# Kernel optimization log

Hardware: AMD Instinct MI355X
Metric: run time of the kernel (lower is better)

## Reference

```python
import jax, jax.numpy as jnp
import numpy as np

N, S, D = 512, 64, 128   # num_nodes, seq_len, model_size
H, K = 4, 32             # num_heads, key_size
E = 4096                 # num_edges
WF = 4                   # widening_factor
EPS = 1e-5


def _alibi(num_heads, seq_len):
    slopes = 2.0 ** (-8.0 * (jnp.arange(1, num_heads + 1, dtype=jnp.float32) / num_heads))
    pos = jnp.arange(seq_len, dtype=jnp.float32)
    rel = pos[None, :] - pos[:, None]  # T - t, <= 0 in causal region
    return (slopes[:, None, None] * rel)[None]  # [1,H,S,S]


def layer_norm(x, scale, offset):
    mu = jnp.mean(x, axis=-1, keepdims=True)
    var = jnp.var(x, axis=-1, keepdims=True)
    return (x - mu) * jax.lax.rsqrt(var + EPS) * scale + offset


def segment_softmax(logits, seg, num_segments):
    maxs = jax.ops.segment_max(logits, seg, num_segments=num_segments)
    e = jnp.exp(logits - maxs[seg])
    denom = jax.ops.segment_sum(e, seg, num_segments=num_segments)
    return e / denom[seg]


def setup_inputs() -> dict:
    key = jax.random.key(0)
    ks = jax.random.split(key, 24)
    sd = 0.02
    inp = {
        'nodes': jax.random.normal(ks[0], (N, S, D), jnp.float32),
        'senders': jax.random.randint(ks[1], (E,), 0, N, jnp.int32),
        'receivers': jax.random.randint(ks[2], (E,), 0, N, jnp.int32),
        'alibi_mask': _alibi(H, S),
        'ln1_s': jnp.ones((D,)), 'ln1_b': jnp.zeros((D,)),
        'wq': jax.random.normal(ks[3], (D, H * K)) * sd, 'bq': jnp.zeros((H * K,)),
        'wk': jax.random.normal(ks[4], (D, H * K)) * sd, 'bk': jnp.zeros((H * K,)),
        'wv': jax.random.normal(ks[5], (D, H * K)) * sd, 'bv': jnp.zeros((H * K,)),
        'wo': jax.random.normal(ks[6], (H * K, D)) * sd, 'bo': jnp.zeros((D,)),
        'ln2_s': jnp.ones((D,)), 'ln2_b': jnp.zeros((D,)),
        'w1': jax.random.normal(ks[7], (D, WF * D)) * sd, 'b1': jnp.zeros((WF * D,)),
        'w2': jax.random.normal(ks[8], (WF * D, D)) * sd, 'b2': jnp.zeros((D,)),
        'ln3_s': jnp.ones((D,)), 'ln3_b': jnp.zeros((D,)),
        'w_sa': jax.random.normal(ks[9], (2 * D, D)) * sd, 'b_sa': jnp.zeros((D,)),
        'w_sq': jax.random.normal(ks[10], (D, H * D)) * sd, 'b_sq': jnp.zeros((H * D,)),
    }
    return inp


def reference(nodes, senders, receivers, alibi_mask,
              ln1_s, ln1_b, wq, bq, wk, bk, wv, bv, wo, bo,
              ln2_s, ln2_b, w1, b1, w2, b2, ln3_s, ln3_b,
              w_sa, b_sa, w_sq, b_sq):
    n, s, d = nodes.shape
    # --- node self-attention with ALiBi + causal mask ---
    xn = layer_norm(nodes, ln1_s, ln1_b)
    q = (xn @ wq + bq).reshape(n, s, H, K)
    k = (xn @ wk + bk).reshape(n, s, H, K)
    v = (xn @ wv + bv).reshape(n, s, H, K)
    logits = jnp.einsum('nthk,nThk->nhtT', q, k)
    logits = alibi_mask + logits / jnp.sqrt(jnp.float32(K))
    causal = jnp.tril(jnp.ones((1, 1, s, s), dtype=bool))
    logits = jnp.where(causal, logits, -1e30)
    w = jax.nn.softmax(logits, axis=-1)
    attn = jnp.einsum('nhtT,nThk->nthk', w, v).reshape(n, s, H * K)
    nodes = nodes + (attn @ wo + bo)  # dropout rate 0 (eval)
    # --- FFN block ---
    xn = layer_norm(nodes, ln2_s, ln2_b)
    dense = jax.nn.gelu(xn @ w1 + b1) @ w2 + b2
    nodes = layer_norm(nodes + dense, ln3_s, ln3_b)
    # --- graph message passing: gather / segment-softmax / segment-sum ---
    sent = nodes[senders]        # [E,S,D]
    recv = nodes[receivers]      # [E,S,D]
    sl = jnp.concatenate([sent, recv], axis=-1) @ w_sa + b_sa  # [E,S,D]
    aw = segment_softmax(sl, receivers, n)                     # [E,S,D]
    sq = (aw @ w_sq + b_sq).reshape(E, s, H, d)                # [E,S,H,D]
    messages = jnp.mean(sq * sent[:, :, None, :], axis=2)      # [E,S,D]
    out = jax.ops.segment_sum(messages, receivers, num_segments=n)
    return out
```

## Files before the change

### kernel.cpp

```cpp
#include <hip/hip_runtime.h>
#include <hip/hip_bf16.h>

typedef __hip_bfloat16 bf16;
typedef __attribute__((ext_vector_type(8))) __bf16 bf8v;
typedef __attribute__((ext_vector_type(4))) float  f4v;

#define NN 512
#define SSEQ 64
#define DDIM 128
#define HH 4
#define NROWS (NN*SSEQ)
#define EMAX 4096
#define ECH 64

__device__ __forceinline__ float b2f(bf16 x){ return __bfloat162float(x); }
__device__ __forceinline__ bf16 f2b(float x){ return __float2bfloat16(x); }
__device__ __forceinline__ float ldf(float x){ return x; }
__device__ __forceinline__ float ldf(bf16 x){ return b2f(x); }
__device__ __forceinline__ void stf(float* p, float v){ *p = v; }
__device__ __forceinline__ void stf(bf16* p, float v){ *p = f2b(v); }

__device__ __forceinline__ f4v mfma16(bf8v a, bf8v b, f4v c){
  return __builtin_amdgcn_mfma_f32_16x16x32_bf16(a, b, c, 0, 0, 0);
}
__device__ __forceinline__ bf8v ldfrag(const void* p){
  return __builtin_bit_cast(bf8v, *(const int4*)p);
}
__device__ __forceinline__ float gelu_f(float v){
  return 0.5f*v*(1.0f + tanhf(0.7978845608028654f*(v + 0.044715f*v*v*v)));
}

__global__ __launch_bounds__(512) void prep_all_k(
    const float* wq, const float* wk, const float* wv, const float* wo,
    const float* w1, const float* w2, const float* wsa,
    const float* w_sq, const float* b_sq,
    const float* bq, const float* bk, const float* bv,
    const int* __restrict__ receivers,
    bf16* wqkvT, bf16* woT, bf16* w1T, bf16* w2T, bf16* wsaTt,
    bf16* wbarT, float* bbar, float* qkv_bias,
    int* off, int* perm, int* chunk_cnt, int E){
  int b = blockIdx.x, t = threadIdx.x;
  if (b < 832){
    if (t >= 256) return;
    const float* W; bf16* Wt; int K, lN, rel, roff = 0;
    if      (b < 64) { W=wq;  Wt=wqkvT; K=128; lN=7; rel=b;     roff=0;   }
    else if (b <128) { W=wk;  Wt=wqkvT; K=128; lN=7; rel=b-64;  roff=128; }
    else if (b <192) { W=wv;  Wt=wqkvT; K=128; lN=7; rel=b-128; roff=256; }
    else if (b <256) { W=wo;  Wt=woT;   K=128; lN=7; rel=b-192; }
    else if (b <512) { W=w1;  Wt=w1T;   K=128; lN=9; rel=b-256; }
    else if (b <768) { W=w2;  Wt=w2T;   K=512; lN=7; rel=b-512; }
    else             { W=wsa; Wt=wsaTt; K=128; lN=7; rel=b-768; }
    int i = rel*256 + t;
    int k = i >> lN, n = i & ((1<<lN)-1);
    Wt[(size_t)(n+roff)*K + k] = f2b(W[i]);
  } else if (b < 896){
    if (t >= 256) return;
    int i = (b-832)*256 + t;
    int c = i>>7, d = i&127;
    float s = 0.f;
    #pragma unroll
    for (int h=0;h<HH;++h) s += w_sq[(size_t)c*(HH*DDIM) + h*DDIM + d];
    wbarT[d*DDIM + c] = f2b(0.25f*s);
  } else if (b < 898){
    if (t >= 256) return;
    int idx = (b-896)*256 + t;
    if (idx < 128){
      float s = 0.f;
      #pragma unroll
      for (int h=0;h<HH;++h) s += b_sq[h*DDIM + idx];
      bbar[idx] = 0.25f*s;
    } else if (idx < 512){
      int j = idx - 128;
      float v = (j<128) ? bq[j] : (j<256) ? bk[j-128] : bv[j-256];
      qkv_bias[j] = v;
    }
  } else if (b == 898){
    __shared__ int s_cnt[NN];
    s_cnt[t] = 0;
    __syncthreads();
    for (int e=t; e<E; e+=512) atomicAdd(&s_cnt[receivers[e]], 1);
    __syncthreads();
    int deg = s_cnt[t];
    int acc = 0, myrank = 0;
    for (int i=0;i<NN;++i){
      int di = s_cnt[i];
      acc    += (i<t) ? di : 0;
      myrank += ((di > deg) || (di == deg && i < t)) ? 1 : 0;
    }
    off[t] = acc;
    if (t==NN-1) off[NN] = acc + deg;
    perm[myrank] = t;
  } else {
    __shared__ int hc[NN];
    int c = b - 899;
    for (int i=t;i<NN;i+=512) hc[i]=0;
    __syncthreads();
    if (t < ECH){
      int e = c*ECH + t;
      if (e < E) atomicAdd(&hc[receivers[e]], 1);
    }
    __syncthreads();
    for (int i=t;i<NN;i+=512) chunk_cnt[(size_t)c*NN + i] = hc[i];
  }
}

__global__ __launch_bounds__(512) void base_k(const int* __restrict__ off,
    const int* __restrict__ chunk_cnt, int* __restrict__ base, int nch){
  int n = threadIdx.x;
  int run = off[n];
  for (int c=0;c<nch;++c){
    base[(size_t)c*NN + n] = run;
    run += chunk_cnt[(size_t)c*NN + n];
  }
}

__global__ __launch_bounds__(64) void slot_k(const int* __restrict__ senders,
    const int* __restrict__ receivers, const int* __restrict__ base,
    int* __restrict__ slot_snd, int E){
  int t = threadIdx.x, c = blockIdx.x;
  int e = c*ECH + t;
  bool valid = (e < E);
  int r  = valid ? receivers[e] : -1;
  int sd = valid ? senders[e]   : 0;
  int rank = 0;
  #pragma unroll
  for (int i=0;i<64;++i){
    int ri = __shfl(r, i);
    rank += (i < t && ri == r) ? 1 : 0;
  }
  if (valid) slot_snd[base[(size_t)c*NN + r] + rank] = sd;
}

template<typename TIN, typename TOUT>
__global__ __launch_bounds__(256) void ln_k(const TIN* __restrict__ x,
    const float* __restrict__ sc, const float* __restrict__ of,
    TOUT* __restrict__ y){
  int row  = blockIdx.x*4 + (threadIdx.x>>6);
  int lane = threadIdx.x & 63;
  size_t base = (size_t)row*DDIM;
  float v0 = ldf(x[base+lane]);
  float v1 = ldf(x[base+lane+64]);
  float s = v0+v1, q = v0*v0+v1*v1;
  #pragma unroll
  for (int m=1;m<64;m<<=1){ s += __shfl_xor(s,m); q += __shfl_xor(q,m); }
  float mu   = s*(1.0f/DDIM);
  float var  = q*(1.0f/DDIM) - mu*mu;
  float rstd = rsqrtf(var + 1e-5f);
  stf(&y[base+lane],    (v0-mu)*rstd*sc[lane]    + of[lane]);
  stf(&y[base+lane+64], (v1-mu)*rstd*sc[lane+64] + of[lane+64]);
}

template<int KT, int ACT, typename TR, bool RES, bool BIAS>
__global__ __launch_bounds__(256) void gemm_m(const bf16* __restrict__ A,
    const bf16* __restrict__ Wt, const float* __restrict__ bias,
    const TR* __restrict__ R, bf16* __restrict__ C, int N){
  __shared__ bf16 sA[64][72];
  __shared__ bf16 sB[64][72];
  int t = threadIdx.x;
  int bm = blockIdx.x, bn = blockIdx.y;
  int w = t>>6, lane = t&63;
  int wr = w>>1, wc = w&1;
  f4v acc[2][2] = {};
  for (int ks=0; ks<KT; ks+=64){
    #pragma unroll
    for (int p=0;p<2;++p){
      int r = p*32 + (t>>3), cc = (t&7)*8;
      *(int4*)(&sA[r][cc]) = *(const int4*)(A  + (size_t)(bm*64+r)*KT + ks + cc);
      *(int4*)(&sB[r][cc]) = *(const int4*)(Wt + (size_t)(bn*64+r)*KT + ks + cc);
    }
    __syncthreads();
    #pragma unroll
    for (int k0=0;k0<64;k0+=32){
      int kc = k0 + 8*(lane>>4);
      bf8v a0 = ldfrag(&sA[wr*32      + (lane&15)][kc]);
      bf8v a1 = ldfrag(&sA[wr*32 + 16 + (lane&15)][kc]);
      bf8v b0 = ldfrag(&sB[wc*32      + (lane&15)][kc]);
      bf8v b1 = ldfrag(&sB[wc*32 + 16 + (lane&15)][kc]);
      acc[0][0] = mfma16(a0, b0, acc[0][0]);
      acc[0][1] = mfma16(a0, b1, acc[0][1]);
      acc[1][0] = mfma16(a1, b0, acc[1][0]);
      acc[1][1] = mfma16(a1, b1, acc[1][1]);
    }
    __syncthreads();
  }
  #pragma unroll
  for (int j=0;j<2;++j){
    int gcol = bn*64 + wc*32 + j*16 + (lane&15);
    float bs = BIAS ? bias[gcol] : 0.f;
    #pragma unroll
    for (int i=0;i<2;++i){
      #pragma unroll
      for (int r=0;r<4;++r){
        int grow = bm*64 + wr*32 + i*16 + 4*(lane>>4) + r;
        float v = acc[i][j][r] + bs;
        if (ACT==1) v = gelu_f(v);
        if (ACT==2) v = __expf(v);
        if (RES) v += ldf(R[(size_t)grow*N + gcol]);
        C[(size_t)grow*N + gcol] = f2b(v);
      }
    }
  }
}

__global__ __launch_bounds__(256) void gemm_wo_ln2_k(const bf16* __restrict__ A,
    const bf16* __restrict__ Wt, const float* __restrict__ bias,
    const float* __restrict__ Rres, const float* __restrict__ lns,
    const float* __restrict__ lnb, bf16* __restrict__ n2out,
    bf16* __restrict__ xnout){
  __shared__ bf16 sA[64][72];
  __shared__ bf16 sB[128][72];
  __shared__ float s_st[2][2][32][2];
  int t = threadIdx.x, bm = blockIdx.x;
  int w = t>>6, lane = t&63, ls = lane&15, lg = lane>>4;
  int wr = w>>1, wc = w&1;
  f4v acc[2][4] = {};
  for (int ks=0; ks<128; ks+=64){
    #pragma unroll
    for (int p=0;p<2;++p){
      int r = p*32 + (t>>3), cc = (t&7)*8;
      *(int4*)(&sA[r][cc]) = *(const int4*)(A + (size_t)(bm*64+r)*128 + ks + cc);
    }
    #pragma unroll
    for (int p=0;p<4;++p){
      int r = p*32 + (t>>3), cc = (t&7)*8;
      *(int4*)(&sB[r][cc]) = *(const int4*)(Wt + (size_t)r*128 + ks + cc);
    }
    __syncthreads();
    #pragma unroll
    for (int k0=0;k0<64;k0+=32){
      int kc = k0 + 8*lg;
      bf8v a0 = ldfrag(&sA[wr*32      + ls][kc]);
      bf8v a1 = ldfrag(&sA[wr*32 + 16 + ls][kc]);
      #pragma unroll
      for (int j=0;j<4;++j){
        bf8v bj = ldfrag(&sB[wc*64 + j*16 + ls][kc]);
        acc[0][j] = mfma16(a0, bj, acc[0][j]);
        acc[1][j] = mfma16(a1, bj, acc[1][j]);
      }
    }
    __syncthreads();
  }
  float x[2][4][4];
  float psum[2][4], psq[2][4];
  #pragma unroll
  for (int i=0;i<2;++i)
    #pragma unroll
    for (int r=0;r<4;++r){ psum[i][r]=0.f; psq[i][r]=0.f; }
  #pragma unroll
  for (int i=0;i<2;++i){
    #pragma unroll
    for (int j=0;j<4;++j){
      int col = wc*64 + j*16 + ls;
      float bs = bias[col];
      #pragma unroll
      for (int r=0;r<4;++r){
        int row = bm*64 + wr*32 + i*16 + 4*lg + r;
        float v = acc[i][j][r] + bs + Rres[(size_t)row*128 + col];
        x[i][j][r] = v;
        psum[i][r] += v;
        psq[i][r]  += v*v;
        n2out[(size_t)row*128 + col] = f2b(v);
      }
    }
  }
  #pragma unroll
  for (int i=0;i<2;++i)
    #pragma unroll
    for (int r=0;r<4;++r){
      float s_=psum[i][r], q_=psq[i][r];
      s_ += __shfl_xor(s_,1); s_ += __shfl_xor(s_,2);
      s_ += __shfl_xor(s_,4); s_ += __shfl_xor(s_,8);
      q_ += __shfl_xor(q_,1); q_ += __shfl_xor(q_,2);
      q_ += __shfl_xor(q_,4); q_ += __shfl_xor(q_,8);
      if (ls == 0){
        int rl = i*16 + 4*lg + r;
        s_st[wr][wc][rl][0] = s_;
        s_st[wr][wc][rl][1] = q_;
      }
    }
  __syncthreads();
  #pragma unroll
  for (int i=0;i<2;++i){
    #pragma unroll
    for (int r=0;r<4;++r){
      int rl = i*16 + 4*lg + r;
      float s_ = s_st[wr][0][rl][0] + s_st[wr][1][rl][0];
      float q_ = s_st[wr][0][rl][1] + s_st[wr][1][rl][1];
      float mu = s_*(1.0f/DDIM);
      float var = q_*(1.0f/DDIM) - mu*mu;
      float rstd = rsqrtf(var + 1e-5f);
      int row = bm*64 + wr*32 + rl;
      #pragma unroll
      for (int j=0;j<4;++j){
        int col = wc*64 + j*16 + ls;
        xnout[(size_t)row*128 + col] = f2b((x[i][j][r]-mu)*rstd*lns[col] + lnb[col]);
      }
    }
  }
}

__global__ __launch_bounds__(256) void gemm_w2_tail_k(const bf16* __restrict__ A,
    const bf16* __restrict__ Wt, const float* __restrict__ bias,
    const bf16* __restrict__ Rres, const float* __restrict__ lns,
    const float* __restrict__ lnb, const bf16* __restrict__ wsaT,
    bf16* __restrict__ r2out, bf16* __restrict__ yexpout){
  __shared__ bf16 sA[64][72];
  __shared__ bf16 sB[128][72];
  __shared__ bf16 sY[64][136];
  __shared__ float s_st[2][2][32][2];
  int t = threadIdx.x, bm = blockIdx.x;
  int w = t>>6, lane = t&63, ls = lane&15, lg = lane>>4;
  int wr = w>>1, wc = w&1;
  f4v acc[2][4] = {};
  for (int ks=0; ks<512; ks+=64){
    #pragma unroll
    for (int p=0;p<2;++p){
      int r = p*32 + (t>>3), cc = (t&7)*8;
      *(int4*)(&sA[r][cc]) = *(const int4*)(A + (size_t)(bm*64+r)*512 + ks + cc);
    }
    #pragma unroll
    for (int p=0;p<4;++p){
      int r = p*32 + (t>>3), cc = (t&7)*8;
      *(int4*)(&sB[r][cc]) = *(const int4*)(Wt + (size_t)r*512 + ks + cc);
    }
    __syncthreads();
    #pragma unroll
    for (int k0=0;k0<64;k0+=32){
      int kc = k0 + 8*lg;
      bf8v a0 = ldfrag(&sA[wr*32      + ls][kc]);
      bf8v a1 = ldfrag(&sA[wr*32 + 16 + ls][kc]);
      #pragma unroll
      for (int j=0;j<4;++j){
        bf8v bj = ldfrag(&sB[wc*64 + j*16 + ls][kc]);
        acc[0][j] = mfma16(a0, bj, acc[0][j]);
        acc[1][j] = mfma16(a1, bj, acc[1][j]);
      }
    }
    __syncthreads();
  }
  float x[2][4][4];
  float psum[2][4], psq[2][4];
  #pragma unroll
  for (int i=0;i<2;++i)
    #pragma unroll
    for (int r=0;r<4;++r){ psum[i][r]=0.f; psq[i][r]=0.f; }
  #pragma unroll
  for (int i=0;i<2;++i){
    #pragma unroll
    for (int j=0;j<4;++j){
      int col = wc*64 + j*16 + ls;
      float bs = bias[col];
      #pragma unroll
      for (int r=0;r<4;++r){
        int row = bm*64 + wr*32 + i*16 + 4*lg + r;
        float v = acc[i][j][r] + bs + b2f(Rres[(size_t)row*128 + col]);
        x[i][j][r] = v;
        psum[i][r] += v;
        psq[i][r]  += v*v;
      }
    }
  }
  #pragma unroll
  for (int i=0;i<2;++i)
    #pragma unroll
    for (int r=0;r<4;++r){
      float s_=psum[i][r], q_=psq[i][r];
      s_ += __shfl_xor(s_,1); s_ += __shfl_xor(s_,2);
      s_ += __shfl_xor(s_,4); s_ += __shfl_xor(s_,8);
      q_ += __shfl_xor(q_,1); q_ += __shfl_xor(q_,2);
      q_ += __shfl_xor(q_,4); q_ += __shfl_xor(q_,8);
      if (ls == 0){
        int rl = i*16 + 4*lg + r;
        s_st[wr][wc][rl][0] = s_;
        s_st[wr][wc][rl][1] = q_;
      }
    }
  __syncthreads();
  #pragma unroll
  for (int i=0;i<2;++i){
    #pragma unroll
    for (int r=0;r<4;++r){
      int rl = i*16 + 4*lg + r;
      float s_ = s_st[wr][0][rl][0] + s_st[wr][1][rl][0];
      float q_ = s_st[wr][0][rl][1] + s_st[wr][1][rl][1];
      float mu = s_*(1.0f/DDIM);
      float var = q_*(1.0f/DDIM) - mu*mu;
      float rstd = rsqrtf(var + 1e-5f);
      int row = bm*64 + wr*32 + rl;
      #pragma unroll
      for (int j=0;j<4;++j){
        int col = wc*64 + j*16 + ls;
        bf16 yb = f2b((x[i][j][r]-mu)*rstd*lns[col] + lnb[col]);
        r2out[(size_t)row*128 + col] = yb;
        sY[wr*32 + rl][col] = yb;
      }
    }
  }
  __syncthreads();
  f4v acc2[2][4] = {};
  for (int ks2=0; ks2<128; ks2+=64){
    #pragma unroll
    for (int p=0;p<4;++p){
      int r = p*32 + (t>>3), cc = (t&7)*8;
      *(int4*)(&sB[r][cc]) = *(const int4*)(wsaT + (size_t)r*128 + ks2 + cc);
    }
    __syncthreads();
    #pragma unroll
    for (int k0=0;k0<64;k0+=32){
      int kc = k0 + 8*lg;
      bf8v a0 = ldfrag(&sY[wr*32      + ls][ks2 + kc]);
      bf8v a1 = ldfrag(&sY[wr*32 + 16 + ls][ks2 + kc]);
      #pragma unroll
      for (int j=0;j<4;++j){
        bf8v bj = ldfrag(&sB[wc*64 + j*16 + ls][kc]);
        acc2[0][j] = mfma16(a0, bj, acc2[0][j]);
        acc2[1][j] = mfma16(a1, bj, acc2[1][j]);
      }
    }
    __syncthreads();
  }
  #pragma unroll
  for (int i=0;i<2;++i){
    #pragma unroll
    for (int j=0;j<4;++j){
      int col = wc*64 + j*16 + ls;
      #pragma unroll
      for (int r=0;r<4;++r){
        int row = bm*64 + wr*32 + i*16 + 4*lg + r;
        yexpout[(size_t)row*128 + col] = f2b(__expf(acc2[i][j][r]));
      }
    }
  }
}

__global__ __launch_bounds__(256) void attn_m(const bf16* __restrict__ qkvb,
    bf16* __restrict__ ob){
  __shared__ bf16 sVT[128][72];
  __shared__ bf16 sP[4][64][72];
  int t = threadIdx.x, n = blockIdx.x;
  int w = t>>6, lane = t&63, ls = lane&15, lg = lane>>4;
  const bf16* qbase = qkvb + (size_t)n*SSEQ*(3*DDIM);
  bf8v qf[4], kf[4];
  #pragma unroll
  for (int mi=0;mi<4;++mi)
    qf[mi] = ldfrag(qbase + (size_t)(16*mi + ls)*(3*DDIM) + 32*w + 8*lg);
  #pragma unroll
  for (int ni=0;ni<4;++ni)
    kf[ni] = ldfrag(qbase + (size_t)(16*ni + ls)*(3*DDIM) + DDIM + 32*w + 8*lg);
  for (int id = t; id < 1024; id += 256){
    int T = id>>4, c = id&15;
    int4 v = *(const int4*)(qbase + (size_t)T*(3*DDIM) + 2*DDIM + c*8);
    const bf16* pv = (const bf16*)&v;
    #pragma unroll
    for (int j=0;j<8;++j){
      int d = c*8 + j;
      sVT[d][T ^ (((d>>3)&7)<<3)] = pv[j];
    }
  }
  f4v accS[4][4];
  #pragma unroll
  for (int mi=0;mi<4;++mi)
    #pragma unroll
    for (int ni=0;ni<4;++ni){
      f4v z = {};
      accS[mi][ni] = mfma16(qf[mi], kf[ni], z);
    }
  __syncthreads();
  const float scale = 0.17677669529663687f;
  const float slope = 1.0f / (float)(4 << (2*w));
  float den[4][4];
  #pragma unroll
  for (int mi=0;mi<4;++mi)
    #pragma unroll
    for (int r=0;r<4;++r) den[mi][r] = 0.f;
  #pragma unroll
  for (int mi=0;mi<4;++mi){
    #pragma unroll
    for (int ni=0;ni<4;++ni){
      #pragma unroll
      for (int r=0;r<4;++r){
        int rel = (16*ni + ls) - (16*mi + 4*lg + r);
        float p = (rel <= 0) ? __expf(accS[mi][ni][r]*scale + slope*(float)rel) : 0.f;
        accS[mi][ni][r] = p;
        den[mi][r] += p;
      }
    }
  }
  #pragma unroll
  for (int mi=0;mi<4;++mi)
    #pragma unroll
    for (int r=0;r<4;++r){
      float d_ = den[mi][r];
      d_ += __shfl_xor(d_, 1);  d_ += __shfl_xor(d_, 2);
      d_ += __shfl_xor(d_, 4);  d_ += __shfl_xor(d_, 8);
      den[mi][r] = 1.0f / d_;
    }
  #pragma unroll
  for (int mi=0;mi<4;++mi)
    #pragma unroll
    for (int ni=0;ni<4;++ni)
      #pragma unroll
      for (int r=0;r<4;++r)
        sP[w][16*mi + 4*lg + r][16*ni + ls] = f2b(accS[mi][ni][r]*den[mi][r]);
  f4v oacc[4][2] = {};
  #pragma unroll
  for (int ks=0;ks<2;++ks){
    bf8v vf[2];
    #pragma unroll
    for (int ni2=0;ni2<2;++ni2){
      int d = 32*w + 16*ni2 + ls;
      vf[ni2] = ldfrag(&sVT[d][(32*ks + 8*lg) ^ (((d>>3)&7)<<3)]);
    }
    #pragma unroll
    for (int mi=0;mi<4;++mi){
      bf8v pa = ldfrag(&sP[w][16*mi + ls][32*ks + 8*lg]);
      #pragma unroll
      for (int ni2=0;ni2<2;++ni2)
        oacc[mi][ni2] = mfma16(pa, vf[ni2], oacc[mi][ni2]);
    }
  }
  #pragma unroll
  for (int mi=0;mi<4;++mi)
    #pragma unroll
    for (int ni2=0;ni2<2;++ni2)
      #pragma unroll
      for (int r=0;r<4;++r)
        ob[(size_t)(n*SSEQ + 16*mi + 4*lg + r)*DDIM + 32*w + 16*ni2 + ls]
          = f2b(oacc[mi][ni2][r]);
}

__global__ __launch_bounds__(128) void msg4_k(const bf16* __restrict__ yexp,
    const bf16* __restrict__ nodes3, const int* __restrict__ off,
    const int* __restrict__ slot_snd, const int* __restrict__ perm,
    const bf16* __restrict__ wbarT, const float* __restrict__ bbar,
    float* __restrict__ out){
  __shared__ bf16  s_sent[2][3][16][72];
  __shared__ float s_den[16][132];
  int t = threadIdx.x, sc = blockIdx.y;
  int n = perm[blockIdx.x];
  int w = t>>6, lane = t&63, ls = lane&15, lg = lane>>4;
  int off0 = off[n], deg = off[n+1]-off0;
  int srow = sc*16 + ls;
  if (deg == 0){
    #pragma unroll
    for (int ct=0;ct<4;++ct)
      #pragma unroll
      for (int r=0;r<4;++r)
        out[((size_t)n*SSEQ + sc*16 + 4*lg + r)*DDIM + w*64 + ct*16 + ls] = 0.f;
    return;
  }
  bf8v B[4][4];
  #pragma unroll
  for (int ct=0;ct<4;++ct)
    #pragma unroll
    for (int kb=0;kb<4;++kb)
      B[ct][kb] = ldfrag(wbarT + (size_t)(w*64 + ct*16 + ls)*DDIM + kb*32 + lg*8);
  float bb[4];
  #pragma unroll
  for (int ct=0;ct<4;++ct) bb[ct] = bbar[w*64 + ct*16 + ls];
  float den[4][8];
  #pragma unroll
  for (int kb=0;kb<4;++kb)
    #pragma unroll
    for (int j=0;j<8;++j) den[kb][j] = 0.f;
  {
    int k = w;
    for (; k+2 < deg; k += 4){
      int s0 = slot_snd[off0+k], s1 = slot_snd[off0+k+2];
      const bf16* y0 = yexp + ((size_t)s0*SSEQ + srow)*DDIM + lg*8;
      const bf16* y1 = yexp + ((size_t)s1*SSEQ + srow)*DDIM + lg*8;
      int4 v0[4], v1[4];
      #pragma unroll
      for (int kb=0;kb<4;++kb) v0[kb] = *(const int4*)(y0 + kb*32);
      #pragma unroll
      for (int kb=0;kb<4;++kb) v1[kb] = *(const int4*)(y1 + kb*32);
      #pragma unroll
      for (int kb=0;kb<4;++kb){
        const bf16* a = (const bf16*)&v0[kb];
        const bf16* b = (const bf16*)&v1[kb];
        #pragma unroll
        for (int j=0;j<8;++j) den[kb][j] += b2f(a[j]) + b2f(b[j]);
      }
    }
    if (k < deg){
      int s0 = slot_snd[off0+k];
      const bf16* y0 = yexp + ((size_t)s0*SSEQ + srow)*DDIM + lg*8;
      #pragma unroll
      for (int kb=0;kb<4;++kb){
        int4 v = *(const int4*)(y0 + kb*32);
        const bf16* a = (const bf16*)&v;
        #pragma unroll
        for (int j=0;j<8;++j) den[kb][j] += b2f(a[j]);
      }
    }
  }
  int l0 = lane*2, l1 = lane*2 + 1;
  int r0 = l0>>3, c0 = (l0&7)*8;
  int r1 = l1>>3, c1 = (l1&7)*8;
  int4 yvA[4], yvB[4], yvC[4];
  {
    int snd = slot_snd[off0];
    const bf16* yr = yexp + ((size_t)snd*SSEQ + srow)*DDIM + lg*8;
    #pragma unroll
    for (int kb=0;kb<4;++kb) yvA[kb] = *(const int4*)(yr + kb*32);
    const bf16* sp = nodes3 + ((size_t)snd*SSEQ + sc*16)*DDIM + w*64;
    *(int4*)&s_sent[w][0][r0][c0] = *(const int4*)(sp + (size_t)r0*DDIM + c0);
    *(int4*)&s_sent[w][0][r1][c1] = *(const int4*)(sp + (size_t)r1*DDIM + c1);
  }
  if (deg > 1){
    int snd = slot_snd[off0+1];
    const bf16* yr = yexp + ((size_t)snd*SSEQ + srow)*DDIM + lg*8;
    #pragma unroll
    for (int kb=0;kb<4;++kb) yvB[kb] = *(const int4*)(yr + kb*32);
    const bf16* sp = nodes3 + ((size_t)snd*SSEQ + sc*16)*DDIM + w*64;
    *(int4*)&s_sent[w][1][r0][c0] = *(const int4*)(sp + (size_t)r0*DDIM + c0);
    *(int4*)&s_sent[w][1][r1][c1] = *(const int4*)(sp + (size_t)r1*DDIM + c1);
  }
  #pragma unroll
  for (int kb=0;kb<4;++kb) yvC[kb] = yvA[kb];
  if (w == 1){
    #pragma unroll
    for (int kb=0;kb<4;++kb)
      #pragma unroll
      for (int j=0;j<8;++j)
        s_den[ls][kb*32 + lg*8 + j] = den[kb][j];
  }
  __syncthreads();
  if (w == 0){
    #pragma unroll
    for (int kb=0;kb<4;++kb)
      #pragma unroll
      for (int j=0;j<8;++j){
        int c = kb*32 + lg*8 + j;
        den[kb][j] = 1.0f / (den[kb][j] + s_den[ls][c]);
        s_den[ls][c] = den[kb][j];
      }
  }
  __syncthreads();
  if (w == 1){
    #pragma unroll
    for (int kb=0;kb<4;++kb)
      #pragma unroll
      for (int j=0;j<8;++j)
        den[kb][j] = s_den[ls][kb*32 + lg*8 + j];
  }
  f4v oacc[4] = {};
  for (int k=0;k<deg;++k){
    if (k+2 < deg){
      int snd2 = slot_snd[off0+k+2];
      const bf16* yr2 = yexp + ((size_t)snd2*SSEQ + srow)*DDIM + lg*8;
      #pragma unroll
      for (int kb=0;kb<4;++kb) yvC[kb] = *(const int4*)(yr2 + kb*32);
      const bf16* sp = nodes3 + ((size_t)snd2*SSEQ + sc*16)*DDIM + w*64;
      int buf2 = (k+2)%3;
      *(int4*)&s_sent[w][buf2][r0][c0] = *(const int4*)(sp + (size_t)r0*DDIM + c0);
      *(int4*)&s_sent[w][buf2][r1][c1] = *(const int4*)(sp + (size_t)r1*DDIM + c1);
    }
    bf8v af[4];
    #pragma unroll
    for (int kb=0;kb<4;++kb){
      const bf16* xv = (const bf16*)&yvA[kb];
      __bf16 tmp[8];
      #pragma unroll
      for (int j=0;j<8;++j){
        bf16 hb_ = f2b(b2f(xv[j]) * den[kb][j]);
        tmp[j] = *(__bf16*)&hb_;
      }
      af[kb] = *(bf8v*)tmp;
    }
    f4v g[4] = {};
    #pragma unroll
    for (int kb=0;kb<4;++kb)
      #pragma unroll
      for (int ct=0;ct<4;++ct)
        g[ct] = mfma16(af[kb], B[ct][kb], g[ct]);
    int buf = k%3;
    #pragma unroll
    for (int ct=0;ct<4;++ct)
      #pragma unroll
      for (int r=0;r<4;++r){
        float sent = b2f(s_sent[w][buf][4*lg + r][ct*16 + ls]);
        oacc[ct][r] += (g[ct][r] + bb[ct]) * sent;
      }
    #pragma unroll
    for (int kb=0;kb<4;++kb){ yvA[kb] = yvB[kb]; yvB[kb] = yvC[kb]; }
  }
  #pragma unroll
  for (int ct=0;ct<4;++ct)
    #pragma unroll
    for (int r=0;r<4;++r)
      out[((size_t)n*SSEQ + sc*16 + 4*lg + r)*DDIM + w*64 + ct*16 + ls] = oacc[ct][r];
}

extern "C" void kernel_launch(void* const* d_in, const int* in_sizes, int n_in,
                              void* d_out, int out_size, void* d_ws, size_t ws_size,
                              hipStream_t stream){
  const float* nodes = (const float*)d_in[0];
  const int*  senders   = (const int*)d_in[1];
  const int*  receivers = (const int*)d_in[2];
  const float* ln1_s=(const float*)d_in[4];  const float* ln1_b=(const float*)d_in[5];
  const float* wq=(const float*)d_in[6];     const float* bq=(const float*)d_in[7];
  const float* wk=(const float*)d_in[8];     const float* bk=(const float*)d_in[9];
  const float* wv=(const float*)d_in[10];    const float* bv_=(const float*)d_in[11];
  const float* wo=(const float*)d_in[12];    const float* bo=(const float*)d_in[13];
  const float* ln2_s=(const float*)d_in[14]; const float* ln2_b=(const float*)d_in[15];
  const float* w1=(const float*)d_in[16];    const float* b1=(const float*)d_in[17];
  const float* w2=(const float*)d_in[18];    const float* b2=(const float*)d_in[19];
  const float* ln3_s=(const float*)d_in[20]; const float* ln3_b=(const float*)d_in[21];
  const float* w_sa=(const float*)d_in[22];
  const float* w_sq=(const float*)d_in[24];  const float* b_sq=(const float*)d_in[25];
  int E = in_sizes[1];
  int nch = (E + ECH - 1)/ECH;

  const size_t MB = 1024*1024;
  char* ws = (char*)d_ws;
  bf16* xn      = (bf16*)(ws);
  bf16* qkvb    = (bf16*)(ws +  8*MB);
  bf16* n2      = (bf16*)(ws + 32*MB);
  bf16* xn2     = (bf16*)(ws + 48*MB);
  bf16* hb      = (bf16*)(ws);
  bf16* attnout = xn;
  bf16* r2     = (bf16*)(ws + 64*MB);
  bf16* yexp   = (bf16*)(ws + 72*MB);
  char* tail = ws + 88*MB;
  bf16*  wbarT   = (bf16*)tail;                       tail += DDIM*DDIM*2;
  float* bbar    = (float*)tail;                      tail += DDIM*4 + 512;
  float* qkv_bias= (float*)tail;                      tail += 3*DDIM*4;
  int*   off     = (int*)tail;                        tail += (NN+8)*4;
  int*   slot_snd= (int*)tail;                        tail += EMAX*4;
  int*   perm    = (int*)tail;                        tail += NN*4;
  int*   ccnt    = (int*)tail;                        tail += 64*NN*4;
  int*   cbase   = (int*)tail;                        tail += 64*NN*4;
  bf16*  wqkvT   = (bf16*)tail;                       tail += 384*128*2;
  bf16*  woT     = (bf16*)tail;                       tail += 128*128*2;
  bf16*  w1T     = (bf16*)tail;                       tail += 128*512*2;
  bf16*  w2T     = (bf16*)tail;                       tail += 512*128*2;
  bf16*  wsaTt   = (bf16*)tail;                       tail += 128*128*2;

  prep_all_k<<<899+nch,512,0,stream>>>(wq,wk,wv,wo,w1,w2,w_sa,w_sq,b_sq,bq,bk,bv_,
                                       receivers,
                                       wqkvT,woT,w1T,w2T,wsaTt,wbarT,bbar,qkv_bias,
                                       off, perm, ccnt, E);
  base_k<<<1,512,0,stream>>>(off, ccnt, cbase, nch);
  slot_k<<<nch,64,0,stream>>>(senders, receivers, cbase, slot_snd, E);

  ln_k<float,bf16><<<NROWS/4,256,0,stream>>>(nodes, ln1_s, ln1_b, xn);
  gemm_m<128,0,float,false,true><<<dim3(NROWS/64,6),256,0,stream>>>(xn, wqkvT, qkv_bias, (const float*)nullptr, qkvb, 384);
  attn_m<<<NN,256,0,stream>>>(qkvb, attnout);
  gemm_wo_ln2_k<<<NROWS/64,256,0,stream>>>(attnout, woT, bo, nodes, ln2_s, ln2_b, n2, xn2);
  gemm_m<128,1,bf16,false,true><<<dim3(NROWS/64,8),256,0,stream>>>(xn2, w1T, b1, (const bf16*)nullptr, hb, 512);
  gemm_w2_tail_k<<<NROWS/64,256,0,stream>>>(hb, w2T, b2, n2, ln3_s, ln3_b, wsaTt, r2, yexp);

  msg4_k<<<dim3(NN,4),128,0,stream>>>(yexp, r2, off, slot_snd, perm, wbarT, bbar, (float*)d_out);
}
```

Measured before the change: 168.5 us.

## Split message kernel across four waves with shared normalized-score tile

The message-passing kernel now runs 256 threads per block. Each of the four waves owns 32 output columns instead of 64, which cuts per-thread weight fragments and accumulators. Each thread loads and normalizes one 8-element slice of the 16x128 score tile per edge and stages it in double-buffered shared memory, replacing per-wave redundant 128-wide row loads. The denominator is computed cooperatively with no cross-wave reduction. The cost is a block-wide barrier every edge iteration and more threads per block.

```diff
diff --git a/kernel.cpp b/kernel.cpp
--- a/kernel.cpp
+++ b/kernel.cpp
@@ -529,167 +529,122 @@
           = f2b(oacc[mi][ni2][r]);
 }
 
-__global__ __launch_bounds__(128) void msg4_k(const bf16* __restrict__ yexp,
+__global__ __launch_bounds__(256) void msg4_k(const bf16* __restrict__ yexp,
     const bf16* __restrict__ nodes3, const int* __restrict__ off,
     const int* __restrict__ slot_snd, const int* __restrict__ perm,
     const bf16* __restrict__ wbarT, const float* __restrict__ bbar,
     float* __restrict__ out){
-  __shared__ bf16  s_sent[2][3][16][72];
-  __shared__ float s_den[16][132];
+  __shared__ bf16 sP[2][16][136];
+  __shared__ bf16 s_sent[4][3][16][36];
   int t = threadIdx.x, sc = blockIdx.y;
   int n = perm[blockIdx.x];
   int w = t>>6, lane = t&63, ls = lane&15, lg = lane>>4;
   int off0 = off[n], deg = off[n+1]-off0;
-  int srow = sc*16 + ls;
+  int dbase = w*32;
   if (deg == 0){
     #pragma unroll
-    for (int ct=0;ct<4;++ct)
+    for (int ct=0;ct<2;++ct)
       #pragma unroll
       for (int r=0;r<4;++r)
-        out[((size_t)n*SSEQ + sc*16 + 4*lg + r)*DDIM + w*64 + ct*16 + ls] = 0.f;
+        out[((size_t)n*SSEQ + sc*16 + 4*lg + r)*DDIM + dbase + ct*16 + ls] = 0.f;
     return;
   }
-  bf8v B[4][4];
-  #pragma unroll
-  for (int ct=0;ct<4;++ct)
+  bf8v B[2][4];
+  #pragma unroll
+  for (int ct=0;ct<2;++ct)
     #pragma unroll
     for (int kb=0;kb<4;++kb)
-      B[ct][kb] = ldfrag(wbarT + (size_t)(w*64 + ct*16 + ls)*DDIM + kb*32 + lg*8);
-  float bb[4];
-  #pragma unroll
-  for (int ct=0;ct<4;++ct) bb[ct] = bbar[w*64 + ct*16 + ls];
-  float den[4][8];
-  #pragma unroll
-  for (int kb=0;kb<4;++kb)
-    #pragma unroll
-    for (int j=0;j<8;++j) den[kb][j] = 0.f;
+      B[ct][kb] = ldfrag(wbarT + (size_t)(dbase + ct*16 + ls)*DDIM + kb*32 + lg*8);
+  float bb[2];
+  #pragma unroll
+  for (int ct=0;ct<2;++ct) bb[ct] = bbar[dbase + ct*16 + ls];
+  int rp = t>>4, cp = (t&15)*8;
+  size_t prow = ((size_t)(sc*16 + rp))*DDIM + cp;
+  float den8[8];
+  #pragma unroll
+  for (int j=0;j<8;++j) den8[j] = 0.f;
   {
-    int k = w;
-    for (; k+2 < deg; k += 4){
-      int s0 = slot_snd[off0+k], s1 = slot_snd[off0+k+2];
-      const bf16* y0 = yexp + ((size_t)s0*SSEQ + srow)*DDIM + lg*8;
-      const bf16* y1 = yexp + ((size_t)s1*SSEQ + srow)*DDIM + lg*8;
-      int4 v0[4], v1[4];
-      #pragma unroll
-      for (int kb=0;kb<4;++kb) v0[kb] = *(const int4*)(y0 + kb*32);
-      #pragma unroll
-      for (int kb=0;kb<4;++kb) v1[kb] = *(const int4*)(y1 + kb*32);
-      #pragma unroll
-      for (int kb=0;kb<4;++kb){
-        const bf16* a = (const bf16*)&v0[kb];
-        const bf16* b = (const bf16*)&v1[kb];
-        #pragma unroll
-        for (int j=0;j<8;++j) den[kb][j] += b2f(a[j]) + b2f(b[j]);
-      }
+    int k = 0;
+    for (; k+2<=deg; k+=2){
+      int s0 = slot_snd[off0+k], s1 = slot_snd[off0+k+1];
+      int4 v0 = *(const int4*)(yexp + (size_t)s0*SSEQ*DDIM + prow);
+      int4 v1 = *(const int4*)(yexp + (size_t)s1*SSEQ*DDIM + prow);
+      const bf16* a = (const bf16*)&v0;
+      const bf16* b = (const bf16*)&v1;
+      #pragma unroll
+      for (int j=0;j<8;++j) den8[j] += b2f(a[j]) + b2f(b[j]);
     }
     if (k < deg){
       int s0 = slot_snd[off0+k];
-      const bf16* y0 = yexp + ((size_t)s0*SSEQ + srow)*DDIM + lg*8;
-      #pragma unroll
-      for (int kb=0;kb<4;++kb){
-        int4 v = *(const int4*)(y0 + kb*32);
-        const bf16* a = (const bf16*)&v;
-        #pragma unroll
-        for (int j=0;j<8;++j) den[kb][j] += b2f(a[j]);
-      }
-    }
-  }
-  int l0 = lane*2, l1 = lane*2 + 1;
-  int r0 = l0>>3, c0 = (l0&7)*8;
-  int r1 = l1>>3, c1 = (l1&7)*8;
-  int4 yvA[4], yvB[4], yvC[4];
+      int4 v = *(const int4*)(yexp + (size_t)s0*SSEQ*DDIM + prow);
+      const bf16* a = (const bf16*)&v;
+      #pragma unroll
+      for (int j=0;j<8;++j) den8[j] += b2f(a[j]);
+    }
+  }
+  #pragma unroll
+  for (int j=0;j<8;++j) den8[j] = 1.0f/den8[j];
+  int rs = lane>>2, cs = (lane&3)*8;
+  int4 yvP[1]; int4 yv1;
   {
     int snd = slot_snd[off0];
-    const bf16* yr = yexp + ((size_t)snd*SSEQ + srow)*DDIM + lg*8;
-    #pragma unroll
-    for (int kb=0;kb<4;++kb) yvA[kb] = *(const int4*)(yr + kb*32);
-    const bf16* sp = nodes3 + ((size_t)snd*SSEQ + sc*16)*DDIM + w*64;
-    *(int4*)&s_sent[w][0][r0][c0] = *(const int4*)(sp + (size_t)r0*DDIM + c0);
-    *(int4*)&s_sent[w][0][r1][c1] = *(const int4*)(sp + (size_t)r1*DDIM + c1);
+    int4 v = *(const int4*)(yexp + (size_t)snd*SSEQ*DDIM + prow);
+    const bf16* a = (const bf16*)&v;
+    bf16 pv[8];
+    #pragma unroll
+    for (int j=0;j<8;++j) pv[j] = f2b(b2f(a[j]) * den8[j]);
+    *(int4*)&sP[0][rp][cp] = *(const int4*)pv;
+    *(int4*)&s_sent[w][0][rs][cs] =
+      *(const int4*)(nodes3 + ((size_t)snd*SSEQ + sc*16 + rs)*DDIM + dbase + cs);
   }
   if (deg > 1){
     int snd = slot_snd[off0+1];
-    const bf16* yr = yexp + ((size_t)snd*SSEQ + srow)*DDIM + lg*8;
-    #pragma unroll
-    for (int kb=0;kb<4;++kb) yvB[kb] = *(const int4*)(yr + kb*32);
-    const bf16* sp = nodes3 + ((size_t)snd*SSEQ + sc*16)*DDIM + w*64;
-    *(int4*)&s_sent[w][1][r0][c0] = *(const int4*)(sp + (size_t)r0*DDIM + c0);
-    *(int4*)&s_sent[w][1][r1][c1] = *(const int4*)(sp + (size_t)r1*DDIM + c1);
-  }
-  #pragma unroll
-  for (int kb=0;kb<4;++kb) yvC[kb] = yvA[kb];
-  if (w == 1){
-    #pragma unroll
-    for (int kb=0;kb<4;++kb)
-      #pragma unroll
-      for (int j=0;j<8;++j)
-        s_den[ls][kb*32 + lg*8 + j] = den[kb][j];
+    yv1 = *(const int4*)(yexp + (size_t)snd*SSEQ*DDIM + prow);
+    *(int4*)&s_sent[w][1][rs][cs] =
+      *(const int4*)(nodes3 + ((size_t)snd*SSEQ + sc*16 + rs)*DDIM + dbase + cs);
   }
   __syncthreads();
-  if (w == 0){
-    #pragma unroll
-    for (int kb=0;kb<4;++kb)
-      #pragma unroll
-      for (int j=0;j<8;++j){
-        int c = kb*32 + lg*8 + j;
-        den[kb][j] = 1.0f / (den[kb][j] + s_den[ls][c]);
-        s_den[ls][c] = den[kb][j];
-      }
-  }
-  __syncthreads();
-  if (w == 1){
-    #pragma unroll
-    for (int kb=0;kb<4;++kb)
-      #pragma unroll
-      for (int j=0;j<8;++j)
-        den[kb][j] = s_den[ls][kb*32 + lg*8 + j];
-  }
-  f4v oacc[4] = {};
+  f4v oacc[2] = {};
+  int4 yvN;
   for (int k=0;k<deg;++k){
+    int buf = k&1;
     if (k+2 < deg){
       int snd2 = slot_snd[off0+k+2];
-      const bf16* yr2 = yexp + ((size_t)snd2*SSEQ + srow)*DDIM + lg*8;
-      #pragma unroll
-      for (int kb=0;kb<4;++kb) yvC[kb] = *(const int4*)(yr2 + kb*32);
-      const bf16* sp = nodes3 + ((size_t)snd2*SSEQ + sc*16)*DDIM + w*64;
-      int buf2 = (k+2)%3;
-      *(int4*)&s_sent[w][buf2][r0][c0] = *(const int4*)(sp + (size_t)r0*DDIM + c0);
-      *(int4*)&s_sent[w][buf2][r1][c1] = *(const int4*)(sp + (size_t)r1*DDIM + c1);
-    }
-    bf8v af[4];
-    #pragma unroll
-    for (int kb=0;kb<4;++kb){
-      const bf16* xv = (const bf16*)&yvA[kb];
-      __bf16 tmp[8];
-      #pragma unroll
-      for (int j=0;j<8;++j){
-        bf16 hb_ = f2b(b2f(xv[j]) * den[kb][j]);
-        tmp[j] = *(__bf16*)&hb_;
-      }
-      af[kb] = *(bf8v*)tmp;
-    }
-    f4v g[4] = {};
+      yvN = *(const int4*)(yexp + (size_t)snd2*SSEQ*DDIM + prow);
+      *(int4*)&s_sent[w][(k+2)%3][rs][cs] =
+        *(const int4*)(nodes3 + ((size_t)snd2*SSEQ + sc*16 + rs)*DDIM + dbase + cs);
+    }
+    if (k+1 < deg){
+      const bf16* a = (const bf16*)&yv1;
+      bf16 pv[8];
+      #pragma unroll
+      for (int j=0;j<8;++j) pv[j] = f2b(b2f(a[j]) * den8[j]);
+      *(int4*)&sP[buf^1][rp][cp] = *(const int4*)pv;
+    }
+    bf8v a4[4];
+    #pragma unroll
+    for (int kb=0;kb<4;++kb) a4[kb] = ldfrag(&sP[buf][ls][kb*32 + lg*8]);
+    f4v g[2] = {};
     #pragma unroll
     for (int kb=0;kb<4;++kb)
       #pragma unroll
-      for (int ct=0;ct<4;++ct)
-        g[ct] = mfma16(af[kb], B[ct][kb], g[ct]);
-    int buf = k%3;
-    #pragma unroll
-    for (int ct=0;ct<4;++ct)
+      for (int ct=0;ct<2;++ct)
+        g[ct] = mfma16(a4[kb], B[ct][kb], g[ct]);
+    #pragma unroll
+    for (int ct=0;ct<2;++ct)
       #pragma unroll
       for (int r=0;r<4;++r){
-        float sent = b2f(s_sent[w][buf][4*lg + r][ct*16 + ls]);
+        float sent = b2f(s_sent[w][k%3][4*lg + r][ct*16 + ls]);
         oacc[ct][r] += (g[ct][r] + bb[ct]) * sent;
       }
-    #pragma unroll
-    for (int kb=0;kb<4;++kb){ yvA[kb] = yvB[kb]; yvB[kb] = yvC[kb]; }
-  }
-  #pragma unroll
-  for (int ct=0;ct<4;++ct)
+    __syncthreads();
+    yv1 = yvN;
+  }
+  #pragma unroll
+  for (int ct=0;ct<2;++ct)
     #pragma unroll
     for (int r=0;r<4;++r)
-      out[((size_t)n*SSEQ + sc*16 + 4*lg + r)*DDIM + w*64 + ct*16 + ls] = oacc[ct][r];
+      out[((size_t)n*SSEQ + sc*16 + 4*lg + r)*DDIM + dbase + ct*16 + ls] = oacc[ct][r];
 }
 
 extern "C" void kernel_launch(void* const* d_in, const int* in_sizes, int n_in,
@@ -751,5 +706,5 @@
   gemm_m<128,1,bf16,false,true><<<dim3(NROWS/64,8),256,0,stream>>>(xn2, w1T, b1, (const bf16*)nullptr, hb, 512);
   gemm_w2_tail_k<<<NROWS/64,256,0,stream>>>(hb, w2T, b2, n2, ln3_s, ln3_b, wsaTt, r2, yexp);
 
-  msg4_k<<<dim3(NN,4),128,0,stream>>>(yexp, r2, off, slot_snd, perm, wbarT, bbar, (float*)d_out);
-}
+  msg4_k<<<dim3(NN,4),256,0,stream>>>(yexp, r2, off, slot_snd, perm, wbarT, bbar, (float*)d_out);
+}
```

Result: faster. 152.4 us (-9.6%).
